# Kernel tuning notes

Hardware: AMD Instinct MI355X
Metric: run time of the kernel (lower is better)

## Reference

```python
import jax, jax.numpy as jnp
import numpy as np

B_, H, N, D = 512, 8, 256, 16   # windows*batch, heads, tokens/window, head_dim
NW = 64                          # windows per image (B_ = 8 images * 64 windows)
TABLE = 961                      # (2*16-1)^2 relative position table rows
EPS = 1e-12                      # F.normalize eps


def setup_inputs() -> dict:
    key = jax.random.key(0)
    k_q, k_k, k_v, k_t, k_i, k_m = jax.random.split(key, 6)
    return {
        "q": jax.random.normal(k_q, (B_, H, N, D), dtype=jnp.float32),
        "k": jax.random.normal(k_k, (B_, H, N, D), dtype=jnp.float32),
        "v": jax.random.normal(k_v, (B_, H, N, D), dtype=jnp.float32),
        "table": jax.random.normal(k_t, (TABLE, H), dtype=jnp.float32),
        "index": jax.random.randint(k_i, (N * N,), 0, TABLE, dtype=jnp.int64),
        "mask": jax.random.normal(k_m, (NW, N, N), dtype=jnp.float32),
    }


def _l2norm(x):
    # matches F.normalize(x, dim=-1): x / max(||x||2, eps)
    n = jnp.sqrt(jnp.sum(x * x, axis=-1, keepdims=True))
    return x / jnp.maximum(n, EPS)


def reference(q, k, v, table, index, mask):
    b, h, n, d = q.shape
    # cosine-normalized QK^T: [B_, H, N, N]
    attn = jnp.einsum("bhnd,bhmd->bhnm", _l2norm(q), _l2norm(k))
    # relative position bias gather: table[index] -> (N*N, H) -> (H, N, N)
    bias = table[index].reshape(n, n, h).transpose(2, 0, 1)
    attn = attn + bias[None]
    # per-window additive mask
    nw = mask.shape[0]
    attn = attn.reshape(b // nw, nw, h, n, n) + mask[None, :, None]
    attn = attn.reshape(b, h, n, n)
    attn = jax.nn.softmax(attn, axis=-1)   # attn_drop is identity at p=0
    x = jnp.einsum("bhnm,bhmd->bhnd", attn, v)
    # transpose(1,2).reshape(B_, N, H*head_dim)
    return x.transpose(0, 2, 1, 3).reshape(b, n, h * d)
```

## Files before the change

kernel.cpp:

```cpp
#include <hip/hip_runtime.h>
#include <stdint.h>

#define HH 8
#define NN 256
#define DD 16
#define NWIN 64
#define LOG2E 1.44269504088896340736f

typedef __attribute__((ext_vector_type(8))) short short8;
typedef __attribute__((ext_vector_type(4))) short short4_t;
typedef __attribute__((ext_vector_type(4))) float f32x4;

static __device__ __forceinline__ unsigned short f2bf(float f) {
    union { float f; uint32_t u; } v; v.f = f;
    uint32_t u = v.u;
    uint32_t r = (u + 0x7fffu + ((u >> 16) & 1u)) >> 16;
    return (unsigned short)r;
}
static __device__ __forceinline__ float bf2f(uint32_t s) {
    union { uint32_t u; float f; } v; v.u = s << 16;
    return v.f;
}
static __device__ __forceinline__ uint32_t pack_bf16_rn(float a, float b) {
    union { float f; uint32_t u; } x, y; x.f = a; y.f = b;
    return __builtin_amdgcn_perm(y.u + 0x8000u, x.u + 0x8000u, 0x07060302u);
}

__global__ void bias_perm_kernel(const float* __restrict__ table,
                                 const int* __restrict__ index,
                                 unsigned short* __restrict__ biasD) {
    int o = blockIdx.x * 256 + threadIdx.x;
    int r  = o & 3;
    int c  = (o >> 2) & 15;
    int qq = (o >> 6) & 3;
    int jt = (o >> 8) & 15;
    int it = (o >> 12) & 15;
    int h  = o >> 16;
    int i = it * 16 + c;
    int j = jt * 16 + qq * 4 + r;
    int idx = index[i * NN + j];
    biasD[o] = f2bf(table[idx * HH + h] * LOG2E);
}

__global__ void mask_perm_kernel(const float* __restrict__ mask,
                                 unsigned short* __restrict__ maskD) {
    __shared__ float lds[16 * 256];
    int w  = blockIdx.x >> 4;
    int it = blockIdx.x & 15;
    int tid = threadIdx.x;
    const float* src = mask + ((size_t)w * NN + it * 16) * NN;
    {
        int row = tid >> 4, col0 = (tid & 15) * 16;
        const float4* s4 = (const float4*)(src + row * NN + col0);
        float4* d4 = (float4*)(lds + row * 256 + col0);
        d4[0] = s4[0]; d4[1] = s4[1]; d4[2] = s4[2]; d4[3] = s4[3];
    }
    __syncthreads();
    unsigned short* dst = maskD + (size_t)blockIdx.x * 4096 + tid * 16;
    int base = tid * 16;
#pragma unroll
    for (int e = 0; e < 16; e++) {
        int o  = base + e;
        int r  = o & 3;
        int c  = (o >> 2) & 15;
        int qq = (o >> 6) & 3;
        int jt = (o >> 8) & 15;
        int j  = jt * 16 + qq * 4 + r;
        dst[e] = f2bf(lds[c * 256 + j] * LOG2E);
    }
}

__global__ __launch_bounds__(256, 4) void attn_kernel(
    const float* __restrict__ q, const float* __restrict__ k, const float* __restrict__ v,
    const unsigned short* __restrict__ biasD, const unsigned short* __restrict__ maskD,
    float* __restrict__ out)
{
    int bh = blockIdx.x;
    int b  = bh >> 3;
    int h  = bh & 7;
    int w  = b & (NWIN - 1);
    int tid  = threadIdx.x;
    int lane = tid & 63;
    int wave = tid >> 6;
    int c    = lane & 15;
    int quad = lane >> 4;

    __shared__ unsigned short Kn[256 * 20];
    __shared__ unsigned short Vl[4096];

    const size_t base = (size_t)bh * (NN * DD);

    {
        const float4* kr = (const float4*)(k + base + (size_t)tid * DD);
        float4 a0 = kr[0], a1 = kr[1], a2 = kr[2], a3 = kr[3];
        float x[16] = {a0.x,a0.y,a0.z,a0.w, a1.x,a1.y,a1.z,a1.w,
                       a2.x,a2.y,a2.z,a2.w, a3.x,a3.y,a3.z,a3.w};
        float ss = 0.f;
#pragma unroll
        for (int e = 0; e < 16; e++) ss += x[e] * x[e];
        float sc = 1.0f / fmaxf(sqrtf(ss), 1e-12f);
        unsigned short* dst = &Kn[tid * 20];
#pragma unroll
        for (int e = 0; e < 16; e++) dst[e] = f2bf(x[e] * sc);
    }
    {
        const float4* vr = (const float4*)(v + base + (size_t)tid * DD);
        float4 a0 = vr[0], a1 = vr[1], a2 = vr[2], a3 = vr[3];
        float x[16] = {a0.x,a0.y,a0.z,a0.w, a1.x,a1.y,a1.z,a1.w,
                       a2.x,a2.y,a2.z,a2.w, a3.x,a3.y,a3.z,a3.w};
        int j  = tid;
        int kc = j >> 5, hi = (j >> 4) & 1, qv = (j >> 2) & 3, r = j & 3;
        int jj = hi * 4 + r;
#pragma unroll
        for (int d = 0; d < 16; d++)
            Vl[((kc * 4 + qv) * 16 + d) * 8 + jj] = f2bf(x[d]);
    }
    __syncthreads();

    short8 vf[8];
#pragma unroll
    for (int kc = 0; kc < 8; kc++)
        vf[kc] = *(const short8*)&Vl[((kc * 4 + quad) * 16 + c) * 8];

#pragma unroll 1
    for (int t = 0; t < 4; t++) {
        int it = wave * 4 + t;
        int i0 = it * 16;

        short8 qf = {0,0,0,0,0,0,0,0};
        if (quad < 2) {
            const float4* qr = (const float4*)(q + base + (size_t)(i0 + c) * DD + quad * 8);
            float4 a0 = qr[0], a1 = qr[1];
            float x[8] = {a0.x,a0.y,a0.z,a0.w, a1.x,a1.y,a1.z,a1.w};
            float ss = 0.f;
#pragma unroll
            for (int e = 0; e < 8; e++) ss += x[e] * x[e];
            ss += __shfl_xor(ss, 16);
            float sc = LOG2E / fmaxf(sqrtf(ss), 1e-12f);
#pragma unroll
            for (int e = 0; e < 8; e++) qf[e] = (short)f2bf(x[e] * sc);
        }

        const unsigned short* bD = biasD + (size_t)(h * 16 + it) * 4096 + quad * 64 + c * 4;
        const unsigned short* mD = maskD + (size_t)(w * 16 + it) * 4096 + quad * 64 + c * 4;
        f32x4 acc[16];
#pragma unroll
        for (int jt = 0; jt < 16; jt++) {
            uint2 bu = *(const uint2*)(bD + jt * 256);
            uint2 mu = *(const uint2*)(mD + jt * 256);
            acc[jt][0] = bf2f(bu.x & 0xffffu) + (bf2f(mu.x & 0xffffu) - 16.0f);
            acc[jt][1] = bf2f(bu.x >> 16)     + (bf2f(mu.x >> 16)     - 16.0f);
            acc[jt][2] = bf2f(bu.y & 0xffffu) + (bf2f(mu.y & 0xffffu) - 16.0f);
            acc[jt][3] = bf2f(bu.y >> 16)     + (bf2f(mu.y >> 16)     - 16.0f);
        }

#pragma unroll
        for (int jt = 0; jt < 16; jt++) {
            short8 kf = {0,0,0,0,0,0,0,0};
            if (quad < 2) {
                const unsigned short* kp = &Kn[(jt * 16 + c) * 20 + quad * 8];
                short4_t lo = *(const short4_t*)kp;
                short4_t hi = *(const short4_t*)(kp + 4);
                kf[0]=lo[0]; kf[1]=lo[1]; kf[2]=lo[2]; kf[3]=lo[3];
                kf[4]=hi[0]; kf[5]=hi[1]; kf[6]=hi[2]; kf[7]=hi[3];
            }
            acc[jt] = __builtin_amdgcn_mfma_f32_16x16x32_bf16(kf, qf, acc[jt], 0, 0, 0);
        }

        float s0 = 0.f, s1 = 0.f, s2 = 0.f, s3 = 0.f;
        f32x4 xacc = {0.f, 0.f, 0.f, 0.f};
#pragma unroll
        for (int kc = 0; kc < 8; kc++) {
            float a0 = __builtin_amdgcn_exp2f(acc[kc * 2][0]);
            float a1 = __builtin_amdgcn_exp2f(acc[kc * 2][1]);
            float a2 = __builtin_amdgcn_exp2f(acc[kc * 2][2]);
            float a3 = __builtin_amdgcn_exp2f(acc[kc * 2][3]);
            float b0 = __builtin_amdgcn_exp2f(acc[kc * 2 + 1][0]);
            float b1 = __builtin_amdgcn_exp2f(acc[kc * 2 + 1][1]);
            float b2 = __builtin_amdgcn_exp2f(acc[kc * 2 + 1][2]);
            float b3 = __builtin_amdgcn_exp2f(acc[kc * 2 + 1][3]);
            s0 += a0 + b0;
            s1 += a1 + b1;
            s2 += a2 + b2;
            s3 += a3 + b3;
            union { short8 s8; uint32_t u[4]; } pp;
            pp.u[0] = pack_bf16_rn(a0, a1);
            pp.u[1] = pack_bf16_rn(a2, a3);
            pp.u[2] = pack_bf16_rn(b0, b1);
            pp.u[3] = pack_bf16_rn(b2, b3);
            xacc = __builtin_amdgcn_mfma_f32_16x16x32_bf16(vf[kc], pp.s8, xacc, 0, 0, 0);
        }
        float sum = (s0 + s1) + (s2 + s3);
        sum += __shfl_xor(sum, 16);
        sum += __shfl_xor(sum, 32);
        float rs = __builtin_amdgcn_rcpf(sum);

        float4 val;
        val.x = xacc[0] * rs;
        val.y = xacc[1] * rs;
        val.z = xacc[2] * rs;
        val.w = xacc[3] * rs;
        float4* dst = (float4*)(out + ((size_t)b * NN + (i0 + c)) * (HH * DD) + h * DD + quad * 4);
        *dst = val;
    }
}

extern "C" void kernel_launch(void* const* d_in, const int* in_sizes, int n_in,
                              void* d_out, int out_size, void* d_ws, size_t ws_size,
                              hipStream_t stream) {
    const float* q     = (const float*)d_in[0];
    const float* k     = (const float*)d_in[1];
    const float* v     = (const float*)d_in[2];
    const float* table = (const float*)d_in[3];
    const int*   index = (const int*)d_in[4];
    const float* mask  = (const float*)d_in[5];
    float* out = (float*)d_out;

    unsigned short* biasD = (unsigned short*)d_ws;
    unsigned short* maskD = biasD + (size_t)HH * NN * NN;

    bias_perm_kernel<<<2048, 256, 0, stream>>>(table, index, biasD);
    mask_perm_kernel<<<1024, 256, 0, stream>>>(mask, maskD);
    attn_kernel<<<4096, 256, 0, stream>>>(q, k, v, biasD, maskD, out);
}
```

Baseline: 346.6 us.

## Chunk score tiles, reload V from LDS, remap blocks per XCD, raise occupancy

Processes the 16 score tiles in four chunks of four, so only four accumulator tiles are live at once, and reads V fragments from LDS per use instead of holding eight in registers. Together with raising the launch-bounds occupancy hint from 4 to 6 blocks, this is meant to lower register pressure and allow more resident waves to hide memory latency. It also remaps block indices so each XCD handles a contiguous range of batches, aiming for better L2 reuse of the per-window mask and per-head bias. The cost is extra LDS reads for V and the risk of spills if the compiler cannot fit the tighter register budget.

```diff
diff --git a/kernel.cpp b/kernel.cpp
--- a/kernel.cpp
+++ b/kernel.cpp
@@ -70,15 +70,18 @@
     }
 }
 
-__global__ __launch_bounds__(256, 4) void attn_kernel(
+__global__ __launch_bounds__(256, 6) void attn_kernel(
     const float* __restrict__ q, const float* __restrict__ k, const float* __restrict__ v,
     const unsigned short* __restrict__ biasD, const unsigned short* __restrict__ maskD,
     float* __restrict__ out)
 {
-    int bh = blockIdx.x;
-    int b  = bh >> 3;
-    int h  = bh & 7;
-    int w  = b & (NWIN - 1);
+    int n   = blockIdx.x;
+    int xcd = n & 7;
+    int m   = n >> 3;
+    int h   = m & 7;
+    int b   = (xcd << 6) | (m >> 3);
+    int bh  = b * 8 + h;
+    int w   = b & (NWIN - 1);
     int tid  = threadIdx.x;
     int lane = tid & 63;
     int wave = tid >> 6;
@@ -117,11 +120,6 @@
     }
     __syncthreads();
 
-    short8 vf[8];
-#pragma unroll
-    for (int kc = 0; kc < 8; kc++)
-        vf[kc] = *(const short8*)&Vl[((kc * 4 + quad) * 16 + c) * 8];
-
 #pragma unroll 1
     for (int t = 0; t < 4; t++) {
         int it = wave * 4 + t;
@@ -143,52 +141,57 @@
 
         const unsigned short* bD = biasD + (size_t)(h * 16 + it) * 4096 + quad * 64 + c * 4;
         const unsigned short* mD = maskD + (size_t)(w * 16 + it) * 4096 + quad * 64 + c * 4;
-        f32x4 acc[16];
-#pragma unroll
-        for (int jt = 0; jt < 16; jt++) {
-            uint2 bu = *(const uint2*)(bD + jt * 256);
-            uint2 mu = *(const uint2*)(mD + jt * 256);
-            acc[jt][0] = bf2f(bu.x & 0xffffu) + (bf2f(mu.x & 0xffffu) - 16.0f);
-            acc[jt][1] = bf2f(bu.x >> 16)     + (bf2f(mu.x >> 16)     - 16.0f);
-            acc[jt][2] = bf2f(bu.y & 0xffffu) + (bf2f(mu.y & 0xffffu) - 16.0f);
-            acc[jt][3] = bf2f(bu.y >> 16)     + (bf2f(mu.y >> 16)     - 16.0f);
-        }
-
-#pragma unroll
-        for (int jt = 0; jt < 16; jt++) {
-            short8 kf = {0,0,0,0,0,0,0,0};
-            if (quad < 2) {
-                const unsigned short* kp = &Kn[(jt * 16 + c) * 20 + quad * 8];
-                short4_t lo = *(const short4_t*)kp;
-                short4_t hi = *(const short4_t*)(kp + 4);
-                kf[0]=lo[0]; kf[1]=lo[1]; kf[2]=lo[2]; kf[3]=lo[3];
-                kf[4]=hi[0]; kf[5]=hi[1]; kf[6]=hi[2]; kf[7]=hi[3];
-            }
-            acc[jt] = __builtin_amdgcn_mfma_f32_16x16x32_bf16(kf, qf, acc[jt], 0, 0, 0);
-        }
 
         float s0 = 0.f, s1 = 0.f, s2 = 0.f, s3 = 0.f;
         f32x4 xacc = {0.f, 0.f, 0.f, 0.f};
 #pragma unroll
-        for (int kc = 0; kc < 8; kc++) {
-            float a0 = __builtin_amdgcn_exp2f(acc[kc * 2][0]);
-            float a1 = __builtin_amdgcn_exp2f(acc[kc * 2][1]);
-            float a2 = __builtin_amdgcn_exp2f(acc[kc * 2][2]);
-            float a3 = __builtin_amdgcn_exp2f(acc[kc * 2][3]);
-            float b0 = __builtin_amdgcn_exp2f(acc[kc * 2 + 1][0]);
-            float b1 = __builtin_amdgcn_exp2f(acc[kc * 2 + 1][1]);
-            float b2 = __builtin_amdgcn_exp2f(acc[kc * 2 + 1][2]);
-            float b3 = __builtin_amdgcn_exp2f(acc[kc * 2 + 1][3]);
-            s0 += a0 + b0;
-            s1 += a1 + b1;
-            s2 += a2 + b2;
-            s3 += a3 + b3;
-            union { short8 s8; uint32_t u[4]; } pp;
-            pp.u[0] = pack_bf16_rn(a0, a1);
-            pp.u[1] = pack_bf16_rn(a2, a3);
-            pp.u[2] = pack_bf16_rn(b0, b1);
-            pp.u[3] = pack_bf16_rn(b2, b3);
-            xacc = __builtin_amdgcn_mfma_f32_16x16x32_bf16(vf[kc], pp.s8, xacc, 0, 0, 0);
+        for (int ch = 0; ch < 4; ch++) {
+            f32x4 acc[4];
+#pragma unroll
+            for (int u = 0; u < 4; u++) {
+                int jt = ch * 4 + u;
+                uint2 bu = *(const uint2*)(bD + jt * 256);
+                uint2 mu = *(const uint2*)(mD + jt * 256);
+                acc[u][0] = bf2f(bu.x & 0xffffu) + (bf2f(mu.x & 0xffffu) - 16.0f);
+                acc[u][1] = bf2f(bu.x >> 16)     + (bf2f(mu.x >> 16)     - 16.0f);
+                acc[u][2] = bf2f(bu.y & 0xffffu) + (bf2f(mu.y & 0xffffu) - 16.0f);
+                acc[u][3] = bf2f(bu.y >> 16)     + (bf2f(mu.y >> 16)     - 16.0f);
+            }
+#pragma unroll
+            for (int u = 0; u < 4; u++) {
+                int jt = ch * 4 + u;
+                union { short8 v; short4_t h4[2]; } kf;
+                kf.v = (short8){0,0,0,0,0,0,0,0};
+                if (quad < 2) {
+                    const unsigned short* kp = &Kn[(jt * 16 + c) * 20 + quad * 8];
+                    kf.h4[0] = *(const short4_t*)kp;
+                    kf.h4[1] = *(const short4_t*)(kp + 4);
+                }
+                acc[u] = __builtin_amdgcn_mfma_f32_16x16x32_bf16(kf.v, qf, acc[u], 0, 0, 0);
+            }
+#pragma unroll
+            for (int half = 0; half < 2; half++) {
+                int kc = ch * 2 + half;
+                float a0 = __builtin_amdgcn_exp2f(acc[half * 2][0]);
+                float a1 = __builtin_amdgcn_exp2f(acc[half * 2][1]);
+                float a2 = __builtin_amdgcn_exp2f(acc[half * 2][2]);
+                float a3 = __builtin_amdgcn_exp2f(acc[half * 2][3]);
+                float b0 = __builtin_amdgcn_exp2f(acc[half * 2 + 1][0]);
+                float b1 = __builtin_amdgcn_exp2f(acc[half * 2 + 1][1]);
+                float b2 = __builtin_amdgcn_exp2f(acc[half * 2 + 1][2]);
+                float b3 = __builtin_amdgcn_exp2f(acc[half * 2 + 1][3]);
+                s0 += a0 + b0;
+                s1 += a1 + b1;
+                s2 += a2 + b2;
+                s3 += a3 + b3;
+                union { short8 s8; uint32_t u[4]; } pp;
+                pp.u[0] = pack_bf16_rn(a0, a1);
+                pp.u[1] = pack_bf16_rn(a2, a3);
+                pp.u[2] = pack_bf16_rn(b0, b1);
+                pp.u[3] = pack_bf16_rn(b2, b3);
+                short8 vfh = *(const short8*)&Vl[((kc * 4 + quad) * 16 + c) * 8];
+                xacc = __builtin_amdgcn_mfma_f32_16x16x32_bf16(vfh, pp.s8, xacc, 0, 0, 0);
+            }
         }
         float sum = (s0 + s1) + (s2 + s3);
         sum += __shfl_xor(sum, 16);
```

Result: slower. 482.4 us (+39.2%).
